# Kernel optimization log

Hardware: AMD Instinct MI355X
Metric: run time of the kernel (lower is better)

## Reference

```python
import jax, jax.numpy as jnp
import numpy as np

D_DEC, D_ENC, H, D_MLP = 1024, 768, 16, 4096
HD = D_DEC // H


def _layernorm(x, w, b, eps=1e-5):
    m = x.mean(-1, keepdims=True)
    v = ((x - m) ** 2).mean(-1, keepdims=True)
    return (x - m) / jnp.sqrt(v + eps) * w + b


def setup_inputs() -> dict:
    key = jax.random.key(0)
    ks = jax.random.split(key, 16)
    B, T, S = 4, 1024, 576

    def lin(k, din, dout):
        kw, kb = jax.random.split(k)
        bound = 1.0 / np.sqrt(din)
        W = jax.random.uniform(kw, (din, dout), jnp.float32, -bound, bound)
        b = jax.random.uniform(kb, (dout,), jnp.float32, -bound, bound)
        return W, b

    qkv_w, qkv_b = lin(ks[0], D_DEC, 3 * D_DEC)
    proj_w, proj_b = lin(ks[1], D_DEC, D_DEC)
    q_w, q_b = lin(ks[2], D_DEC, D_DEC)
    k_w, k_b = lin(ks[3], D_ENC, D_DEC)
    v_w, v_b = lin(ks[4], D_ENC, D_DEC)
    out_w, out_b = lin(ks[5], D_DEC, D_DEC)
    mlp1_w, mlp1_b = lin(ks[6], D_DEC, D_MLP)
    mlp2_w, mlp2_b = lin(ks[7], D_MLP, D_DEC)

    return {
        "x": jax.random.normal(ks[8], (B, T, D_DEC), jnp.float32),
        "enc": jax.random.normal(ks[9], (B, S, D_ENC), jnp.float32),
        "tgt_key_padding_mask": jnp.zeros((B, T), bool),
        "enc_padding_mask": jnp.zeros((B, S), bool),
        "ln1_w": jnp.ones((D_DEC,)), "ln1_b": jnp.zeros((D_DEC,)),
        "qkv_w": qkv_w, "qkv_b": qkv_b, "proj_w": proj_w, "proj_b": proj_b,
        "ln2_w": jnp.ones((D_DEC,)), "ln2_b": jnp.zeros((D_DEC,)),
        "q_w": q_w, "q_b": q_b, "k_w": k_w, "k_b": k_b,
        "v_w": v_w, "v_b": v_b, "out_w": out_w, "out_b": out_b,
        "ln3_w": jnp.ones((D_DEC,)), "ln3_b": jnp.zeros((D_DEC,)),
        "mlp1_w": mlp1_w, "mlp1_b": mlp1_b, "mlp2_w": mlp2_w, "mlp2_b": mlp2_b,
    }


def _decoder_block(x, enc, tgt_mask, enc_mask,
                   ln1_w, ln1_b, qkv_w, qkv_b, proj_w, proj_b,
                   ln2_w, ln2_b, q_w, q_b, k_w, k_b, v_w, v_b, out_w, out_b,
                   ln3_w, ln3_b, mlp1_w, mlp1_b, mlp2_w, mlp2_b):
    B, T, C = x.shape
    S = enc.shape[1]
    scale = HD ** -0.5
    neg = jnp.asarray(-jnp.inf, x.dtype)

    # ---- causal self-attention ----
    h = _layernorm(x, ln1_w, ln1_b)
    qkv = (h @ qkv_w + qkv_b).reshape(B, T, 3, H, HD)
    q, k, v = [qkv[:, :, i].transpose(0, 2, 1, 3) for i in range(3)]  # [B,H,T,HD]
    attn = jnp.einsum("bhtd,bhsd->bhts", q, k) * scale
    causal = jnp.triu(jnp.ones((T, T), bool), 1)
    attn = jnp.where(causal[None, None], neg, attn)
    attn = jnp.where(tgt_mask[:, None, None, :], neg, attn)
    attn = jax.nn.softmax(attn, axis=-1)
    sa = jnp.einsum("bhts,bhsd->bhtd", attn, v).transpose(0, 2, 1, 3).reshape(B, T, C)
    x = x + sa @ proj_w + proj_b

    # ---- cross-attention ----
    h = _layernorm(x, ln2_w, ln2_b)
    q = (h @ q_w + q_b).reshape(B, T, H, HD).transpose(0, 2, 1, 3)
    k = (enc @ k_w + k_b).reshape(B, S, H, HD).transpose(0, 2, 1, 3)
    v = (enc @ v_w + v_b).reshape(B, S, H, HD).transpose(0, 2, 1, 3)
    attn = jnp.einsum("bhtd,bhsd->bhts", q, k) * scale
    attn = jnp.where(enc_mask[:, None, None, :], neg, attn)
    attn = jax.nn.softmax(attn, axis=-1)
    ca = jnp.einsum("bhts,bhsd->bhtd", attn, v).transpose(0, 2, 1, 3).reshape(B, T, C)
    x = x + ca @ out_w + out_b

    # ---- MLP (exact GELU, matching torch nn.GELU default) ----
    h = _layernorm(x, ln3_w, ln3_b)
    h = jax.nn.gelu(h @ mlp1_w + mlp1_b, approximate=False)
    x = x + h @ mlp2_w + mlp2_b
    return x


def reference(x, enc, tgt_key_padding_mask, enc_padding_mask,
              ln1_w, ln1_b, qkv_w, qkv_b, proj_w, proj_b,
              ln2_w, ln2_b, q_w, q_b, k_w, k_b, v_w, v_b, out_w, out_b,
              ln3_w, ln3_b, mlp1_w, mlp1_b, mlp2_w, mlp2_b):
    return _decoder_block(x, enc, tgt_key_padding_mask, enc_padding_mask,
                          ln1_w, ln1_b, qkv_w, qkv_b, proj_w, proj_b,
                          ln2_w, ln2_b, q_w, q_b, k_w, k_b, v_w, v_b, out_w, out_b,
                          ln3_w, ln3_b, mlp1_w, mlp1_b, mlp2_w, mlp2_b)
```

## Files before the change

kernel.cpp:

```cpp
#include <hip/hip_runtime.h>
#include <hip/hip_bf16.h>

typedef unsigned short u16;
typedef __bf16 bf16x8 __attribute__((ext_vector_type(8)));
typedef float f32x4 __attribute__((ext_vector_type(4)));

__device__ __forceinline__ float bf2f(u16 v) { return __uint_as_float(((unsigned)v) << 16); }
__device__ __forceinline__ u16 f2bf(float f) {
  unsigned u = __float_as_uint(f);
  u += 0x7FFFu + ((u >> 16) & 1u);
  return (u16)(u >> 16);
}
__device__ __forceinline__ float gelu_exact(float x) {
  return 0.5f * x * (1.0f + erff(x * 0.70710678118654752f));
}

__device__ __forceinline__ void async_load16(const u16* g, u16* l) {
  __builtin_amdgcn_global_load_lds((const __attribute__((address_space(1))) void*)g,
                                   (__attribute__((address_space(3))) void*)l, 16, 0, 0);
}

__global__ void sniff_kernel(const u16* __restrict__ x, int* __restrict__ flag) {
  int tid = threadIdx.x;
  int hits = 0;
  #pragma unroll
  for (int s = 0; s < 2; ++s) {
    float f = fabsf(bf2f(x[2 * (tid + 64 * s)]));
    hits += (f >= 0.00390625f && f <= 16.0f) ? 1 : 0;
  }
  #pragma unroll
  for (int off = 32; off; off >>= 1) hits += __shfl_xor(hits, off);
  if (tid == 0) flag[0] = (hits >= 64) ? 1 : 0;
}

__global__ __launch_bounds__(256) void in2bf_kernel(const void* __restrict__ src, u16* __restrict__ dst,
                                                    int n4, const int* __restrict__ flagp) {
  int i = blockIdx.x * 256 + threadIdx.x;
  if (i >= n4) return;
  if (*flagp) {
    ((ushort4*)dst)[i] = ((const ushort4*)src)[i];
  } else {
    float4 v = ((const float4*)src)[i];
    ushort4 o; o.x = f2bf(v.x); o.y = f2bf(v.y); o.z = f2bf(v.z); o.w = f2bf(v.w);
    ((ushort4*)dst)[i] = o;
  }
}

__global__ __launch_bounds__(256) void small2bf_kernel(
    const void* s0, const void* s1, const void* s2, const void* s3,
    const void* s4, const void* s5, const void* s6, const void* s7,
    const void* s8, const void* s9, const void* s10, const void* s11,
    const void* s12, const void* s13,
    u16* __restrict__ dst, const int* __restrict__ flagp) {
  const void* srcs[14] = {s0, s1, s2, s3, s4, s5, s6, s7, s8, s9, s10, s11, s12, s13};
  int blk = blockIdx.x;
  int seg, u;
  if (blk < 6)       { seg = blk;            u = 0; }
  else if (blk < 9)  { seg = 6;              u = blk - 6; }
  else if (blk < 14) { seg = 7 + (blk - 9);  u = 0; }
  else if (blk < 18) { seg = 12;             u = blk - 14; }
  else               { seg = 13;             u = 0; }
  const void* src = srcs[seg];
  int i = threadIdx.x + u * 256;
  u16* d = dst + (size_t)blk * 1024;
  if (*flagp) {
    ((ushort4*)d)[threadIdx.x] = ((const ushort4*)src)[i];
  } else {
    float4 v = ((const float4*)src)[i];
    ushort4 o; o.x = f2bf(v.x); o.y = f2bf(v.y); o.z = f2bf(v.z); o.w = f2bf(v.w);
    ((ushort4*)d)[threadIdx.x] = o;
  }
}

__global__ __launch_bounds__(256) void in2f32_kernel(const void* __restrict__ src, float* __restrict__ dst,
                                                     int n4, const int* __restrict__ flagp) {
  int i = blockIdx.x * 256 + threadIdx.x;
  if (i >= n4) return;
  if (*flagp) {
    ushort4 v = ((const ushort4*)src)[i];
    float4 o; o.x = bf2f(v.x); o.y = bf2f(v.y); o.z = bf2f(v.z); o.w = bf2f(v.w);
    ((float4*)dst)[i] = o;
  } else {
    ((float4*)dst)[i] = ((const float4*)src)[i];
  }
}

__global__ __launch_bounds__(256) void transpose_k(const void* __restrict__ in_, u16* __restrict__ out,
                                                   int R, int C, const int* __restrict__ flagp) {
  int flag = *flagp;
  __shared__ u16 tile[32][33];
  int c0 = blockIdx.x * 32, r0 = blockIdx.y * 32;
  int tx = threadIdx.x & 31, ty = threadIdx.x >> 5;
  #pragma unroll
  for (int j = 0; j < 32; j += 8) {
    size_t idx = (size_t)(r0 + ty + j) * C + c0 + tx;
    tile[ty + j][tx] = flag ? ((const u16*)in_)[idx] : f2bf(((const float*)in_)[idx]);
  }
  __syncthreads();
  #pragma unroll
  for (int j = 0; j < 32; j += 8)
    out[(size_t)(c0 + ty + j) * R + r0 + tx] = tile[tx][ty + j];
}

__global__ __launch_bounds__(256) void ln_kernel(const float* __restrict__ x,
                                                 const u16* __restrict__ w, const u16* __restrict__ b,
                                                 u16* __restrict__ out) {
  int row = blockIdx.x, tid = threadIdx.x;
  float4 v = ((const float4*)(x + (size_t)row * 1024))[tid];
  float s = v.x + v.y + v.z + v.w;
  #pragma unroll
  for (int off = 32; off; off >>= 1) s += __shfl_xor(s, off);
  __shared__ float red1[4], red2[4];
  if ((tid & 63) == 0) red1[tid >> 6] = s;
  __syncthreads();
  float mean = (red1[0] + red1[1] + red1[2] + red1[3]) * (1.0f / 1024.0f);
  float d0 = v.x - mean, d1 = v.y - mean, d2 = v.z - mean, d3 = v.w - mean;
  float vs = d0 * d0 + d1 * d1 + d2 * d2 + d3 * d3;
  #pragma unroll
  for (int off = 32; off; off >>= 1) vs += __shfl_xor(vs, off);
  if ((tid & 63) == 0) red2[tid >> 6] = vs;
  __syncthreads();
  float var = (red2[0] + red2[1] + red2[2] + red2[3]) * (1.0f / 1024.0f);
  float rs = rsqrtf(var + 1e-5f);
  int c = tid * 4;
  ushort4 o;
  o.x = f2bf(d0 * rs * bf2f(w[c + 0]) + bf2f(b[c + 0]));
  o.y = f2bf(d1 * rs * bf2f(w[c + 1]) + bf2f(b[c + 1]));
  o.z = f2bf(d2 * rs * bf2f(w[c + 2]) + bf2f(b[c + 2]));
  o.w = f2bf(d3 * rs * bf2f(w[c + 3]) + bf2f(b[c + 3]));
  ((ushort4*)(out + (size_t)row * 1024))[tid] = o;
}

template <int MODE, int TN>
__global__ __launch_bounds__(256) void gemm_tn(const u16* __restrict__ A, const u16* __restrict__ Bt,
                                               const u16* __restrict__ bias,
                                               const float* __restrict__ resid_in, float* __restrict__ resid_out,
                                               void* __restrict__ outp, int M, int N, int K,
                                               const int* __restrict__ flagp) {
  constexpr int NI = TN / 32;
  __shared__ __align__(16) u16 As[128 * 64];
  __shared__ __align__(16) u16 Bs[TN * 64];

  int nwg = gridDim.x * gridDim.y;
  int bid = blockIdx.y * gridDim.x + blockIdx.x;
  int chunk = nwg >> 3;
  int s = (bid & 7) * chunk + (bid >> 3);
  int bx = s % gridDim.x, by = s / gridDim.x;

  int n0 = bx * TN, m0 = by * 128;
  int tid = threadIdx.x;
  int lane = tid & 63, w = tid >> 6;
  int wm = w & 1, wn = w >> 1;
  int quad = lane >> 4, l15 = lane & 15;
  int sw = l15 & 7;
  int flag = (MODE == 3) ? *flagp : 0;
  f32x4 acc[4][NI];
  #pragma unroll
  for (int i = 0; i < 4; i++)
    #pragma unroll
    for (int j = 0; j < NI; j++) acc[i][j] = (f32x4){0.f, 0.f, 0.f, 0.f};

  int srow8 = lane >> 3;
  int scol = ((lane & 7) ^ srow8) * 8;
  const u16* Abase = A + (size_t)(m0 + srow8) * K + scol;
  const u16* Bbase = Bt + (size_t)(n0 + srow8) * K + scol;

  for (int k0 = 0; k0 < K; k0 += 64) {
    #pragma unroll
    for (int j = 0; j < 4; ++j) {
      int r0 = (w * 4 + j) * 8;
      async_load16(Abase + (size_t)r0 * K + k0, &As[r0 * 64]);
    }
    #pragma unroll
    for (int j = 0; j < TN / 32; ++j) {
      int r0 = (w * (TN / 32) + j) * 8;
      async_load16(Bbase + (size_t)r0 * K + k0, &Bs[r0 * 64]);
    }
    __syncthreads();
    #pragma unroll
    for (int kk = 0; kk < 64; kk += 32) {
      int cbase = (kk >> 3) + quad;
      int slot = (cbase ^ sw) << 3;
      bf16x8 af[4], bfr[NI];
      #pragma unroll
      for (int i = 0; i < 4; i++)
        af[i] = *(const bf16x8*)&As[(wm * 64 + i * 16 + l15) * 64 + slot];
      #pragma unroll
      for (int j = 0; j < NI; j++)
        bfr[j] = *(const bf16x8*)&Bs[(wn * (TN / 2) + j * 16 + l15) * 64 + slot];
      #pragma unroll
      for (int mi = 0; mi < 4; mi++)
        #pragma unroll
        for (int ni = 0; ni < NI; ni++)
          acc[mi][ni] = __builtin_amdgcn_mfma_f32_16x16x32_bf16(af[mi], bfr[ni], acc[mi][ni], 0, 0, 0);
    }
    __syncthreads();
  }

  int col_base = n0 + wn * (TN / 2), row_base = m0 + wm * 64;
  #pragma unroll
  for (int mi = 0; mi < 4; mi++) {
    #pragma unroll
    for (int ni = 0; ni < NI; ni++) {
      int col = col_base + ni * 16 + l15;
      float bv = bf2f(bias[col]);
      #pragma unroll
      for (int r = 0; r < 4; r++) {
        int row = row_base + mi * 16 + quad * 4 + r;
        float vv = acc[mi][ni][r] + bv;
        size_t idx = (size_t)row * N + col;
        if (MODE == 0) ((u16*)outp)[idx] = f2bf(vv);
        else if (MODE == 1) resid_out[idx] = resid_in[idx] + vv;
        else if (MODE == 2) ((u16*)outp)[idx] = f2bf(gelu_exact(vv));
        else {
          float ov = resid_in[idx] + vv;
          if (flag) ((u16*)outp)[idx] = f2bf(ov);
          else ((float*)outp)[idx] = ov;
        }
      }
    }
  }
}

__global__ __launch_bounds__(256) void attn_mfma(const u16* __restrict__ Q, const u16* __restrict__ K,
                                                 const u16* __restrict__ V, u16* __restrict__ O,
                                                 int T, int S, int qstride, int kstride, int causal) {
  int bh = blockIdx.y, b = bh >> 4, h = bh & 15;
  int gx = gridDim.x, xi = blockIdx.x;
  int qi = (xi & 1) ? (gx - 1 - (xi >> 1)) : (xi >> 1);
  int qt = qi * 64;

  const u16* Qb = Q + (size_t)b * T * qstride + h * 64;
  const u16* Kb = K + (size_t)b * S * kstride + h * 64;
  const u16* Vb = V + (size_t)b * S * kstride + h * 64;
  u16* Ob = O + (size_t)b * T * 1024 + h * 64;

  int tid = threadIdx.x, lane = tid & 63, w = tid >> 6;
  int quad = lane >> 4, l15 = lane & 15;

  __shared__ __align__(16) u16 Ks[64 * 64];
  __shared__ __align__(16) u16 Vt[64 * 64];
  __shared__ __align__(16) u16 Ps[4][16 * 64];

  int srow8 = lane >> 3;
  int scol = ((lane & 7) ^ srow8) * 8;

  #pragma unroll
  for (int j = 0; j < 2; ++j) {
    int r0 = (w * 2 + j) * 8;
    async_load16(Qb + (size_t)(qt + r0 + srow8) * qstride + scol, &Ks[r0 * 64]);
  }
  asm volatile("" ::: "memory");
  uint4 v0 = *(const uint4*)&Vb[(size_t)lane * kstride + w * 16];
  uint4 v1 = *(const uint4*)&Vb[(size_t)lane * kstride + w * 16 + 8];
  asm volatile("s_waitcnt vmcnt(2)" ::: "memory");
  __builtin_amdgcn_s_barrier();

  int qrow = w * 16 + l15;
  bf16x8 qfrag[2];
  #pragma unroll
  for (int c = 0; c < 2; ++c)
    qfrag[c] = *(const bf16x8*)&Ks[qrow * 64 + (((c * 4 + quad) ^ (l15 & 7)) << 3)];
  asm volatile("s_waitcnt lgkmcnt(0)" ::: "memory");

  float m_i[4], l_i[4];
  f32x4 oacc[4];
  #pragma unroll
  for (int r = 0; r < 4; ++r) { m_i[r] = -1e30f; l_i[r] = 0.f; }
  #pragma unroll
  for (int ni = 0; ni < 4; ++ni) oacc[ni] = (f32x4){0.f, 0.f, 0.f, 0.f};

  int nk = causal ? (qi + 1) * 64 : S;
  int tg0 = qt + w * 16 + quad * 4;

  for (int s0 = 0; s0 < nk; s0 += 64) {
    __builtin_amdgcn_s_barrier();
    #pragma unroll
    for (int j = 0; j < 2; ++j) {
      int r0 = (w * 2 + j) * 8;
      async_load16(Kb + (size_t)(s0 + r0 + srow8) * kstride + scol, &Ks[r0 * 64]);
    }
    asm volatile("" ::: "memory");
    union { uint4 u[2]; u16 e[16]; } vv; vv.u[0] = v0; vv.u[1] = v1;
    #pragma unroll
    for (int j = 0; j < 16; ++j) {
      int d = w * 16 + j;
      Vt[d * 64 + ((((lane >> 3) ^ (j & 7)) << 3) | (lane & 7))] = vv.e[j];
    }
    if (s0 + 64 < nk) {
      v0 = *(const uint4*)&Vb[(size_t)(s0 + 64 + lane) * kstride + w * 16];
      v1 = *(const uint4*)&Vb[(size_t)(s0 + 64 + lane) * kstride + w * 16 + 8];
      asm volatile("s_waitcnt vmcnt(2)" ::: "memory");
    } else {
      asm volatile("s_waitcnt vmcnt(0)" ::: "memory");
    }
    asm volatile("s_waitcnt lgkmcnt(0)" ::: "memory");
    __builtin_amdgcn_s_barrier();

    f32x4 sacc[4];
    #pragma unroll
    for (int ni = 0; ni < 4; ++ni) sacc[ni] = (f32x4){0.f, 0.f, 0.f, 0.f};
    __builtin_amdgcn_s_setprio(1);
    #pragma unroll
    for (int c = 0; c < 2; ++c) {
      #pragma unroll
      for (int ni = 0; ni < 4; ++ni) {
        bf16x8 kf = *(const bf16x8*)&Ks[(ni * 16 + l15) * 64 + (((c * 4 + quad) ^ (l15 & 7)) << 3)];
        sacc[ni] = __builtin_amdgcn_mfma_f32_16x16x32_bf16(qfrag[c], kf, sacc[ni], 0, 0, 0);
      }
    }
    __builtin_amdgcn_s_setprio(0);

    #pragma unroll
    for (int ni = 0; ni < 4; ++ni)
      #pragma unroll
      for (int r = 0; r < 4; ++r) sacc[ni][r] *= 0.125f;
    if (causal && s0 + 63 > qt + w * 16) {
      #pragma unroll
      for (int ni = 0; ni < 4; ++ni) {
        int key = s0 + ni * 16 + l15;
        #pragma unroll
        for (int r = 0; r < 4; ++r)
          if (key > tg0 + r) sacc[ni][r] = -1e30f;
      }
    }

    float mnew[4], alpha[4], psum[4];
    #pragma unroll
    for (int r = 0; r < 4; ++r) {
      float mx = fmaxf(fmaxf(sacc[0][r], sacc[1][r]), fmaxf(sacc[2][r], sacc[3][r]));
      #pragma unroll
      for (int off = 1; off < 16; off <<= 1) mx = fmaxf(mx, __shfl_xor(mx, off));
      mnew[r] = fmaxf(m_i[r], mx);
      alpha[r] = __expf(m_i[r] - mnew[r]);
      m_i[r] = mnew[r];
      psum[r] = 0.f;
    }
    #pragma unroll
    for (int ni = 0; ni < 4; ++ni) {
      #pragma unroll
      for (int r = 0; r < 4; ++r) {
        float p = __expf(sacc[ni][r] - mnew[r]);
        psum[r] += p;
        int row = quad * 4 + r;
        int blk = (ni * 2 + (l15 >> 3)) ^ (row & 7);
        Ps[w][row * 64 + (blk << 3) + (l15 & 7)] = f2bf(p);
      }
    }
    #pragma unroll
    for (int r = 0; r < 4; ++r) {
      float ps = psum[r];
      #pragma unroll
      for (int off = 1; off < 16; off <<= 1) ps += __shfl_xor(ps, off);
      l_i[r] = l_i[r] * alpha[r] + ps;
    }

    bf16x8 pfrag[2];
    #pragma unroll
    for (int c = 0; c < 2; ++c)
      pfrag[c] = *(const bf16x8*)&Ps[w][l15 * 64 + (((c * 4 + quad) ^ (l15 & 7)) << 3)];
    #pragma unroll
    for (int ni = 0; ni < 4; ++ni)
      #pragma unroll
      for (int r = 0; r < 4; ++r) oacc[ni][r] *= alpha[r];
    __builtin_amdgcn_s_setprio(1);
    #pragma unroll
    for (int c = 0; c < 2; ++c) {
      #pragma unroll
      for (int ni = 0; ni < 4; ++ni) {
        bf16x8 vf = *(const bf16x8*)&Vt[(ni * 16 + l15) * 64 + (((c * 4 + quad) ^ (l15 & 7)) << 3)];
        oacc[ni] = __builtin_amdgcn_mfma_f32_16x16x32_bf16(pfrag[c], vf, oacc[ni], 0, 0, 0);
      }
    }
    __builtin_amdgcn_s_setprio(0);
  }

  #pragma unroll
  for (int ni = 0; ni < 4; ++ni) {
    #pragma unroll
    for (int r = 0; r < 4; ++r) {
      int t = tg0 + r;
      int d = ni * 16 + l15;
      Ob[(size_t)t * 1024 + d] = f2bf(oacc[ni][r] / l_i[r]);
    }
  }
}

extern "C" void kernel_launch(void* const* d_in, const int* in_sizes, int n_in,
                              void* d_out, int out_size, void* d_ws, size_t ws_size,
                              hipStream_t stream) {
  const void* x_in   = d_in[0];
  const void* enc_in = d_in[1];
  const void* ln1_w = d_in[4];  const void* ln1_b = d_in[5];
  const void* qkv_w = d_in[6];  const void* qkv_b = d_in[7];
  const void* proj_w = d_in[8]; const void* proj_b = d_in[9];
  const void* ln2_w = d_in[10]; const void* ln2_b = d_in[11];
  const void* q_w = d_in[12];   const void* q_b = d_in[13];
  const void* k_w = d_in[14];   const void* k_b = d_in[15];
  const void* v_w = d_in[16];   const void* v_b = d_in[17];
  const void* out_w = d_in[18]; const void* out_b = d_in[19];
  const void* ln3_w = d_in[20]; const void* ln3_b = d_in[21];
  const void* mlp1_w = d_in[22]; const void* mlp1_b = d_in[23];
  const void* mlp2_w = d_in[24]; const void* mlp2_b = d_in[25];

  char* ws = (char*)d_ws;
  size_t off = 0;
  auto alloc = [&](size_t bytes) { char* p = ws + off; off += (bytes + 255) & ~(size_t)255; return p; };
  float* xf   = (float*)alloc(4096ull * 1024 * 4);
  u16* hb     = (u16*)alloc(4096ull * 1024 * 2);
  u16* big    = (u16*)alloc(4096ull * 4096 * 2);
  u16* wT     = (u16*)alloc(3072ull * 1024 * 2);
  u16* encb   = (u16*)alloc(2304ull * 768 * 2);
  u16* pool   = (u16*)alloc(20480ull * 2);
  int* flag   = (int*)alloc(256);
  (void)ws_size;

  u16* q_bf = big;
  u16* k_bf = big + 4096ull * 1024;
  u16* v_bf = big + (4096ull + 2304) * 1024;

  u16 *p_ln1w = pool, *p_ln1b = pool + 1024, *p_ln2w = pool + 2048, *p_ln2b = pool + 3072;
  u16 *p_ln3w = pool + 4096, *p_ln3b = pool + 5120;
  u16 *p_qkvb = pool + 6144, *p_projb = pool + 9216, *p_qb = pool + 10240, *p_kb = pool + 11264;
  u16 *p_vb = pool + 12288, *p_outb = pool + 13312, *p_m1b = pool + 14336, *p_m2b = pool + 18432;

  sniff_kernel<<<1, 64, 0, stream>>>((const u16*)x_in, flag);
  in2f32_kernel<<<4096, 256, 0, stream>>>(x_in, xf, 1048576, flag);
  in2bf_kernel<<<1728, 256, 0, stream>>>(enc_in, encb, 442368, flag);
  small2bf_kernel<<<19, 256, 0, stream>>>(ln1_w, ln1_b, ln2_w, ln2_b, ln3_w, ln3_b,
                                          qkv_b, proj_b, q_b, k_b, v_b, out_b,
                                          mlp1_b, mlp2_b, pool, flag);

  ln_kernel<<<4096, 256, 0, stream>>>(xf, p_ln1w, p_ln1b, hb);
  transpose_k<<<dim3(96, 32), 256, 0, stream>>>(qkv_w, wT, 1024, 3072, flag);
  gemm_tn<0, 128><<<dim3(24, 32), 256, 0, stream>>>(hb, wT, p_qkvb, nullptr, nullptr, big, 4096, 3072, 1024, flag);
  attn_mfma<<<dim3(16, 64), 256, 0, stream>>>(big, big + 1024, big + 2048, hb, 1024, 1024, 3072, 3072, 1);
  transpose_k<<<dim3(32, 32), 256, 0, stream>>>(proj_w, wT, 1024, 1024, flag);
  gemm_tn<1, 64><<<dim3(16, 32), 256, 0, stream>>>(hb, wT, p_projb, xf, xf, nullptr, 4096, 1024, 1024, flag);

  ln_kernel<<<4096, 256, 0, stream>>>(xf, p_ln2w, p_ln2b, hb);
  transpose_k<<<dim3(32, 32), 256, 0, stream>>>(q_w, wT, 1024, 1024, flag);
  gemm_tn<0, 64><<<dim3(16, 32), 256, 0, stream>>>(hb, wT, p_qb, nullptr, nullptr, q_bf, 4096, 1024, 1024, flag);
  transpose_k<<<dim3(32, 24), 256, 0, stream>>>(k_w, wT, 768, 1024, flag);
  gemm_tn<0, 64><<<dim3(16, 18), 256, 0, stream>>>(encb, wT, p_kb, nullptr, nullptr, k_bf, 2304, 1024, 768, flag);
  transpose_k<<<dim3(32, 24), 256, 0, stream>>>(v_w, wT, 768, 1024, flag);
  gemm_tn<0, 64><<<dim3(16, 18), 256, 0, stream>>>(encb, wT, p_vb, nullptr, nullptr, v_bf, 2304, 1024, 768, flag);
  attn_mfma<<<dim3(16, 64), 256, 0, stream>>>(q_bf, k_bf, v_bf, hb, 1024, 576, 1024, 1024, 0);
  transpose_k<<<dim3(32, 32), 256, 0, stream>>>(out_w, wT, 1024, 1024, flag);
  gemm_tn<1, 64><<<dim3(16, 32), 256, 0, stream>>>(hb, wT, p_outb, xf, xf, nullptr, 4096, 1024, 1024, flag);

  ln_kernel<<<4096, 256, 0, stream>>>(xf, p_ln3w, p_ln3b, hb);
  transpose_k<<<dim3(128, 32), 256, 0, stream>>>(mlp1_w, wT, 1024, 4096, flag);
  gemm_tn<2, 128><<<dim3(32, 32), 256, 0, stream>>>(hb, wT, p_m1b, nullptr, nullptr, big, 4096, 4096, 1024, flag);
  transpose_k<<<dim3(32, 128), 256, 0, stream>>>(mlp2_w, wT, 4096, 1024, flag);
  gemm_tn<3, 64><<<dim3(16, 32), 256, 0, stream>>>(big, wT, p_m2b, xf, nullptr, d_out, 4096, 1024, 4096, flag);
}
```

Before: 589.0 us.

## Process 128 query rows per attention block to reuse K/V tiles

Each attention workgroup now handles two 64-row query blocks (128 rows), so every K and V tile loaded into shared memory serves twice as many queries, halving K/V load and transpose traffic. The grid drops to 8 blocks along x, causal scheduling switches to a diagonal rotation of query tiles, and the first row block is skipped once it is fully masked. This costs more registers (launch bounds set to 2 blocks per SM), a larger P buffer in LDS, and fewer blocks in flight.

```diff
diff --git a/kernel.cpp b/kernel.cpp
--- a/kernel.cpp
+++ b/kernel.cpp
@@ -222,13 +222,13 @@
   }
 }
 
-__global__ __launch_bounds__(256) void attn_mfma(const u16* __restrict__ Q, const u16* __restrict__ K,
-                                                 const u16* __restrict__ V, u16* __restrict__ O,
-                                                 int T, int S, int qstride, int kstride, int causal) {
+__global__ __launch_bounds__(256, 2) void attn_mfma(const u16* __restrict__ Q, const u16* __restrict__ K,
+                                                    const u16* __restrict__ V, u16* __restrict__ O,
+                                                    int T, int S, int qstride, int kstride, int causal) {
   int bh = blockIdx.y, b = bh >> 4, h = bh & 15;
-  int gx = gridDim.x, xi = blockIdx.x;
-  int qi = (xi & 1) ? (gx - 1 - (xi >> 1)) : (xi >> 1);
-  int qt = qi * 64;
+  int x = blockIdx.x, y = blockIdx.y;
+  int qi = causal ? ((x + y) & 7) : x;
+  int qt = qi * 128;
 
   const u16* Qb = Q + (size_t)b * T * qstride + h * 64;
   const u16* Kb = K + (size_t)b * S * kstride + h * 64;
@@ -240,15 +240,15 @@
 
   __shared__ __align__(16) u16 Ks[64 * 64];
   __shared__ __align__(16) u16 Vt[64 * 64];
-  __shared__ __align__(16) u16 Ps[4][16 * 64];
+  __shared__ __align__(16) u16 Ps[128 * 64];
 
   int srow8 = lane >> 3;
   int scol = ((lane & 7) ^ srow8) * 8;
 
   #pragma unroll
-  for (int j = 0; j < 2; ++j) {
-    int r0 = (w * 2 + j) * 8;
-    async_load16(Qb + (size_t)(qt + r0 + srow8) * qstride + scol, &Ks[r0 * 64]);
+  for (int j = 0; j < 4; ++j) {
+    int r0 = (w * 4 + j) * 8;
+    async_load16(Qb + (size_t)(qt + r0 + srow8) * qstride + scol, &Ps[r0 * 64]);
   }
   asm volatile("" ::: "memory");
   uint4 v0 = *(const uint4*)&Vb[(size_t)lane * kstride + w * 16];
@@ -256,22 +256,25 @@
   asm volatile("s_waitcnt vmcnt(2)" ::: "memory");
   __builtin_amdgcn_s_barrier();
 
-  int qrow = w * 16 + l15;
-  bf16x8 qfrag[2];
-  #pragma unroll
-  for (int c = 0; c < 2; ++c)
-    qfrag[c] = *(const bf16x8*)&Ks[qrow * 64 + (((c * 4 + quad) ^ (l15 & 7)) << 3)];
+  bf16x8 qfrag[2][2];
+  #pragma unroll
+  for (int rb = 0; rb < 2; ++rb)
+    #pragma unroll
+    for (int c = 0; c < 2; ++c)
+      qfrag[rb][c] = *(const bf16x8*)&Ps[(rb * 64 + w * 16 + l15) * 64 + (((c * 4 + quad) ^ (l15 & 7)) << 3)];
   asm volatile("s_waitcnt lgkmcnt(0)" ::: "memory");
 
-  float m_i[4], l_i[4];
-  f32x4 oacc[4];
-  #pragma unroll
-  for (int r = 0; r < 4; ++r) { m_i[r] = -1e30f; l_i[r] = 0.f; }
-  #pragma unroll
-  for (int ni = 0; ni < 4; ++ni) oacc[ni] = (f32x4){0.f, 0.f, 0.f, 0.f};
-
-  int nk = causal ? (qi + 1) * 64 : S;
-  int tg0 = qt + w * 16 + quad * 4;
+  float m_i[2][4], l_i[2][4];
+  f32x4 oacc[2][4];
+  #pragma unroll
+  for (int rb = 0; rb < 2; ++rb) {
+    #pragma unroll
+    for (int r = 0; r < 4; ++r) { m_i[rb][r] = -1e30f; l_i[rb][r] = 0.f; }
+    #pragma unroll
+    for (int ni = 0; ni < 4; ++ni) oacc[rb][ni] = (f32x4){0.f, 0.f, 0.f, 0.f};
+  }
+
+  int nk = causal ? (qt + 128) : S;
 
   for (int s0 = 0; s0 < nk; s0 += 64) {
     __builtin_amdgcn_s_barrier();
@@ -297,91 +300,101 @@
     asm volatile("s_waitcnt lgkmcnt(0)" ::: "memory");
     __builtin_amdgcn_s_barrier();
 
-    f32x4 sacc[4];
-    #pragma unroll
-    for (int ni = 0; ni < 4; ++ni) sacc[ni] = (f32x4){0.f, 0.f, 0.f, 0.f};
-    __builtin_amdgcn_s_setprio(1);
-    #pragma unroll
-    for (int c = 0; c < 2; ++c) {
+    #pragma unroll
+    for (int rb = 0; rb < 2; ++rb) {
+      if (rb == 0 && causal && s0 >= qt + 64) continue;
+      int tg0 = qt + rb * 64 + w * 16 + quad * 4;
+
+      f32x4 sacc[4];
+      #pragma unroll
+      for (int ni = 0; ni < 4; ++ni) sacc[ni] = (f32x4){0.f, 0.f, 0.f, 0.f};
+      __builtin_amdgcn_s_setprio(1);
+      #pragma unroll
+      for (int c = 0; c < 2; ++c) {
+        #pragma unroll
+        for (int ni = 0; ni < 4; ++ni) {
+          bf16x8 kf = *(const bf16x8*)&Ks[(ni * 16 + l15) * 64 + (((c * 4 + quad) ^ (l15 & 7)) << 3)];
+          sacc[ni] = __builtin_amdgcn_mfma_f32_16x16x32_bf16(qfrag[rb][c], kf, sacc[ni], 0, 0, 0);
+        }
+      }
+      __builtin_amdgcn_s_setprio(0);
+
+      #pragma unroll
+      for (int ni = 0; ni < 4; ++ni)
+        #pragma unroll
+        for (int r = 0; r < 4; ++r) sacc[ni][r] *= 0.125f;
+      if (causal && s0 + 63 > qt + rb * 64 + w * 16) {
+        #pragma unroll
+        for (int ni = 0; ni < 4; ++ni) {
+          int key = s0 + ni * 16 + l15;
+          #pragma unroll
+          for (int r = 0; r < 4; ++r)
+            if (key > tg0 + r) sacc[ni][r] = -1e30f;
+        }
+      }
+
+      float mnew[4], alpha[4], psum[4];
+      #pragma unroll
+      for (int r = 0; r < 4; ++r) {
+        float mx = fmaxf(fmaxf(sacc[0][r], sacc[1][r]), fmaxf(sacc[2][r], sacc[3][r]));
+        #pragma unroll
+        for (int off = 1; off < 16; off <<= 1) mx = fmaxf(mx, __shfl_xor(mx, off));
+        mnew[r] = fmaxf(m_i[rb][r], mx);
+        alpha[r] = __expf(m_i[rb][r] - mnew[r]);
+        m_i[rb][r] = mnew[r];
+        psum[r] = 0.f;
+      }
       #pragma unroll
       for (int ni = 0; ni < 4; ++ni) {
-        bf16x8 kf = *(const bf16x8*)&Ks[(ni * 16 + l15) * 64 + (((c * 4 + quad) ^ (l15 & 7)) << 3)];
-        sacc[ni] = __builtin_amdgcn_mfma_f32_16x16x32_bf16(qfrag[c], kf, sacc[ni], 0, 0, 0);
-      }
-    }
-    __builtin_amdgcn_s_setprio(0);
-
-    #pragma unroll
-    for (int ni = 0; ni < 4; ++ni)
-      #pragma unroll
-      for (int r = 0; r < 4; ++r) sacc[ni][r] *= 0.125f;
-    if (causal && s0 + 63 > qt + w * 16) {
-      #pragma unroll
-      for (int ni = 0; ni < 4; ++ni) {
-        int key = s0 + ni * 16 + l15;
-        #pragma unroll
-        for (int r = 0; r < 4; ++r)
-          if (key > tg0 + r) sacc[ni][r] = -1e30f;
-      }
-    }
-
-    float mnew[4], alpha[4], psum[4];
-    #pragma unroll
-    for (int r = 0; r < 4; ++r) {
-      float mx = fmaxf(fmaxf(sacc[0][r], sacc[1][r]), fmaxf(sacc[2][r], sacc[3][r]));
-      #pragma unroll
-      for (int off = 1; off < 16; off <<= 1) mx = fmaxf(mx, __shfl_xor(mx, off));
-      mnew[r] = fmaxf(m_i[r], mx);
-      alpha[r] = __expf(m_i[r] - mnew[r]);
-      m_i[r] = mnew[r];
-      psum[r] = 0.f;
-    }
+        #pragma unroll
+        for (int r = 0; r < 4; ++r) {
+          float p = __expf(sacc[ni][r] - mnew[r]);
+          psum[r] += p;
+          int row = quad * 4 + r;
+          int blk = (ni * 2 + (l15 >> 3)) ^ (row & 7);
+          Ps[(w * 32 + rb * 16 + row) * 64 + (blk << 3) + (l15 & 7)] = f2bf(p);
+        }
+      }
+      #pragma unroll
+      for (int r = 0; r < 4; ++r) {
+        float ps = psum[r];
+        #pragma unroll
+        for (int off = 1; off < 16; off <<= 1) ps += __shfl_xor(ps, off);
+        l_i[rb][r] = l_i[rb][r] * alpha[r] + ps;
+      }
+
+      bf16x8 pfrag[2];
+      #pragma unroll
+      for (int c = 0; c < 2; ++c)
+        pfrag[c] = *(const bf16x8*)&Ps[(w * 32 + rb * 16 + l15) * 64 + (((c * 4 + quad) ^ (l15 & 7)) << 3)];
+      #pragma unroll
+      for (int ni = 0; ni < 4; ++ni)
+        #pragma unroll
+        for (int r = 0; r < 4; ++r) oacc[rb][ni][r] *= alpha[r];
+      __builtin_amdgcn_s_setprio(1);
+      #pragma unroll
+      for (int c = 0; c < 2; ++c) {
+        #pragma unroll
+        for (int ni = 0; ni < 4; ++ni) {
+          bf16x8 vf = *(const bf16x8*)&Vt[(ni * 16 + l15) * 64 + (((c * 4 + quad) ^ (l15 & 7)) << 3)];
+          oacc[rb][ni] = __builtin_amdgcn_mfma_f32_16x16x32_bf16(pfrag[c], vf, oacc[rb][ni], 0, 0, 0);
+        }
+      }
+      __builtin_amdgcn_s_setprio(0);
+    }
+  }
+
+  #pragma unroll
+  for (int rb = 0; rb < 2; ++rb) {
+    int tg0 = qt + rb * 64 + w * 16 + quad * 4;
     #pragma unroll
     for (int ni = 0; ni < 4; ++ni) {
       #pragma unroll
       for (int r = 0; r < 4; ++r) {
-        float p = __expf(sacc[ni][r] - mnew[r]);
-        psum[r] += p;
-        int row = quad * 4 + r;
-        int blk = (ni * 2 + (l15 >> 3)) ^ (row & 7);
-        Ps[w][row * 64 + (blk << 3) + (l15 & 7)] = f2bf(p);
-      }
-    }
-    #pragma unroll
-    for (int r = 0; r < 4; ++r) {
-      float ps = psum[r];
-      #pragma unroll
-      for (int off = 1; off < 16; off <<= 1) ps += __shfl_xor(ps, off);
-      l_i[r] = l_i[r] * alpha[r] + ps;
-    }
-
-    bf16x8 pfrag[2];
-    #pragma unroll
-    for (int c = 0; c < 2; ++c)
-      pfrag[c] = *(const bf16x8*)&Ps[w][l15 * 64 + (((c * 4 + quad) ^ (l15 & 7)) << 3)];
-    #pragma unroll
-    for (int ni = 0; ni < 4; ++ni)
-      #pragma unroll
-      for (int r = 0; r < 4; ++r) oacc[ni][r] *= alpha[r];
-    __builtin_amdgcn_s_setprio(1);
-    #pragma unroll
-    for (int c = 0; c < 2; ++c) {
-      #pragma unroll
-      for (int ni = 0; ni < 4; ++ni) {
-        bf16x8 vf = *(const bf16x8*)&Vt[(ni * 16 + l15) * 64 + (((c * 4 + quad) ^ (l15 & 7)) << 3)];
-        oacc[ni] = __builtin_amdgcn_mfma_f32_16x16x32_bf16(pfrag[c], vf, oacc[ni], 0, 0, 0);
-      }
-    }
-    __builtin_amdgcn_s_setprio(0);
-  }
-
-  #pragma unroll
-  for (int ni = 0; ni < 4; ++ni) {
-    #pragma unroll
-    for (int r = 0; r < 4; ++r) {
-      int t = tg0 + r;
-      int d = ni * 16 + l15;
-      Ob[(size_t)t * 1024 + d] = f2bf(oacc[ni][r] / l_i[r]);
+        int t = tg0 + r;
+        int d = ni * 16 + l15;
+        Ob[(size_t)t * 1024 + d] = f2bf(oacc[rb][ni][r] / l_i[rb][r]);
+      }
     }
   }
 }
@@ -434,7 +447,7 @@
   ln_kernel<<<4096, 256, 0, stream>>>(xf, p_ln1w, p_ln1b, hb);
   transpose_k<<<dim3(96, 32), 256, 0, stream>>>(qkv_w, wT, 1024, 3072, flag);
   gemm_tn<0, 128><<<dim3(24, 32), 256, 0, stream>>>(hb, wT, p_qkvb, nullptr, nullptr, big, 4096, 3072, 1024, flag);
-  attn_mfma<<<dim3(16, 64), 256, 0, stream>>>(big, big + 1024, big + 2048, hb, 1024, 1024, 3072, 3072, 1);
+  attn_mfma<<<dim3(8, 64), 256, 0, stream>>>(big, big + 1024, big + 2048, hb, 1024, 1024, 3072, 3072, 1);
   transpose_k<<<dim3(32, 32), 256, 0, stream>>>(proj_w, wT, 1024, 1024, flag);
   gemm_tn<1, 64><<<dim3(16, 32), 256, 0, stream>>>(hb, wT, p_projb, xf, xf, nullptr, 4096, 1024, 1024, flag);
 
@@ -445,7 +458,7 @@
   gemm_tn<0, 64><<<dim3(16, 18), 256, 0, stream>>>(encb, wT, p_kb, nullptr, nullptr, k_bf, 2304, 1024, 768, flag);
   transpose_k<<<dim3(32, 24), 256, 0, stream>>>(v_w, wT, 768, 1024, flag);
   gemm_tn<0, 64><<<dim3(16, 18), 256, 0, stream>>>(encb, wT, p_vb, nullptr, nullptr, v_bf, 2304, 1024, 768, flag);
-  attn_mfma<<<dim3(16, 64), 256, 0, stream>>>(q_bf, k_bf, v_bf, hb, 1024, 576, 1024, 1024, 0);
+  attn_mfma<<<dim3(8, 64), 256, 0, stream>>>(q_bf, k_bf, v_bf, hb, 1024, 576, 1024, 1024, 0);
   transpose_k<<<dim3(32, 32), 256, 0, stream>>>(out_w, wT, 1024, 1024, flag);
   gemm_tn<1, 64><<<dim3(16, 32), 256, 0, stream>>>(hb, wT, p_outb, xf, xf, nullptr, 4096, 1024, 1024, flag);
 
```

Result: no change. 577.5 us (-2.0%).

## Add 256x128 eight-wave GEMM with XCD-aware block remap; remap attention grid

Applied to the files above, without the earlier changes.

Adds a gemm_wide kernel with 512 threads and a 256x128 output tile, which doubles A-tile reuse. Block IDs are remapped so consecutive chunks stay on the same XCD for better L2 locality. It replaces the QKV and MLP1 GEMMs. The attention kernel also gets an XCD-aware mapping that groups heads per chunk, in place of the old alternating causal load-balancing order. The new GEMM has no double buffering and uses a full sync per K step, so latency hiding may suffer, and the attention change may unbalance the causal work.

```diff
diff --git a/kernel.cpp b/kernel.cpp
--- a/kernel.cpp
+++ b/kernel.cpp
@@ -222,12 +222,95 @@
   }
 }
 
+template <int MODE>
+__global__ __launch_bounds__(512) void gemm_wide(const u16* __restrict__ A, const u16* __restrict__ Bt,
+                                                 const u16* __restrict__ bias,
+                                                 void* __restrict__ outp, int M, int N, int K) {
+  __shared__ __align__(16) u16 As[256 * 64];
+  __shared__ __align__(16) u16 Bs[128 * 64];
+
+  int nwg = gridDim.x * gridDim.y;
+  int bid = blockIdx.y * gridDim.x + blockIdx.x;
+  int chunk = nwg >> 3;
+  int s = (bid & 7) * chunk + (bid >> 3);
+  int bx = s % gridDim.x, by = s / gridDim.x;
+
+  int n0 = bx * 128, m0 = by * 256;
+  int tid = threadIdx.x;
+  int lane = tid & 63, w = tid >> 6;
+  int wm = w & 3, wn = w >> 2;
+  int quad = lane >> 4, l15 = lane & 15;
+  int sw = l15 & 7;
+  f32x4 acc[4][4];
+  #pragma unroll
+  for (int i = 0; i < 4; i++)
+    #pragma unroll
+    for (int j = 0; j < 4; j++) acc[i][j] = (f32x4){0.f, 0.f, 0.f, 0.f};
+
+  int srow8 = lane >> 3;
+  int scol = ((lane & 7) ^ srow8) * 8;
+  const u16* Abase = A + (size_t)(m0 + srow8) * K + scol;
+  const u16* Bbase = Bt + (size_t)(n0 + srow8) * K + scol;
+
+  for (int k0 = 0; k0 < K; k0 += 64) {
+    #pragma unroll
+    for (int j = 0; j < 4; ++j) {
+      int r0 = (w * 4 + j) * 8;
+      async_load16(Abase + (size_t)r0 * K + k0, &As[r0 * 64]);
+    }
+    #pragma unroll
+    for (int j = 0; j < 2; ++j) {
+      int r0 = (w * 2 + j) * 8;
+      async_load16(Bbase + (size_t)r0 * K + k0, &Bs[r0 * 64]);
+    }
+    __syncthreads();
+    #pragma unroll
+    for (int kk = 0; kk < 64; kk += 32) {
+      int cbase = (kk >> 3) + quad;
+      int slot = (cbase ^ sw) << 3;
+      bf16x8 af[4], bfr[4];
+      #pragma unroll
+      for (int i = 0; i < 4; i++)
+        af[i] = *(const bf16x8*)&As[(wm * 64 + i * 16 + l15) * 64 + slot];
+      #pragma unroll
+      for (int j = 0; j < 4; j++)
+        bfr[j] = *(const bf16x8*)&Bs[(wn * 64 + j * 16 + l15) * 64 + slot];
+      #pragma unroll
+      for (int mi = 0; mi < 4; mi++)
+        #pragma unroll
+        for (int ni = 0; ni < 4; ni++)
+          acc[mi][ni] = __builtin_amdgcn_mfma_f32_16x16x32_bf16(af[mi], bfr[ni], acc[mi][ni], 0, 0, 0);
+    }
+    __syncthreads();
+  }
+
+  int col_base = n0 + wn * 64, row_base = m0 + wm * 64;
+  #pragma unroll
+  for (int mi = 0; mi < 4; mi++) {
+    #pragma unroll
+    for (int ni = 0; ni < 4; ni++) {
+      int col = col_base + ni * 16 + l15;
+      float bv = bf2f(bias[col]);
+      #pragma unroll
+      for (int r = 0; r < 4; r++) {
+        int row = row_base + mi * 16 + quad * 4 + r;
+        float vv = acc[mi][ni][r] + bv;
+        size_t idx = (size_t)row * N + col;
+        if (MODE == 0) ((u16*)outp)[idx] = f2bf(vv);
+        else ((u16*)outp)[idx] = f2bf(gelu_exact(vv));
+      }
+    }
+  }
+}
+
 __global__ __launch_bounds__(256) void attn_mfma(const u16* __restrict__ Q, const u16* __restrict__ K,
                                                  const u16* __restrict__ V, u16* __restrict__ O,
                                                  int T, int S, int qstride, int kstride, int causal) {
-  int bh = blockIdx.y, b = bh >> 4, h = bh & 15;
-  int gx = gridDim.x, xi = blockIdx.x;
-  int qi = (xi & 1) ? (gx - 1 - (xi >> 1)) : (xi >> 1);
+  int slot = blockIdx.y * gridDim.x + blockIdx.x;
+  int c = slot & 7, u = slot >> 3;
+  int bh = c * 8 + (u >> 4);
+  int qi = u & 15;
+  int b = bh >> 4, h = bh & 15;
   int qt = qi * 64;
 
   const u16* Qb = Q + (size_t)b * T * qstride + h * 64;
@@ -259,8 +342,8 @@
   int qrow = w * 16 + l15;
   bf16x8 qfrag[2];
   #pragma unroll
-  for (int c = 0; c < 2; ++c)
-    qfrag[c] = *(const bf16x8*)&Ks[qrow * 64 + (((c * 4 + quad) ^ (l15 & 7)) << 3)];
+  for (int cc = 0; cc < 2; ++cc)
+    qfrag[cc] = *(const bf16x8*)&Ks[qrow * 64 + (((cc * 4 + quad) ^ (l15 & 7)) << 3)];
   asm volatile("s_waitcnt lgkmcnt(0)" ::: "memory");
 
   float m_i[4], l_i[4];
@@ -281,7 +364,7 @@
       async_load16(Kb + (size_t)(s0 + r0 + srow8) * kstride + scol, &Ks[r0 * 64]);
     }
     asm volatile("" ::: "memory");
-    union { uint4 u[2]; u16 e[16]; } vv; vv.u[0] = v0; vv.u[1] = v1;
+    union { uint4 u4[2]; u16 e[16]; } vv; vv.u4[0] = v0; vv.u4[1] = v1;
     #pragma unroll
     for (int j = 0; j < 16; ++j) {
       int d = w * 16 + j;
@@ -302,11 +385,11 @@
     for (int ni = 0; ni < 4; ++ni) sacc[ni] = (f32x4){0.f, 0.f, 0.f, 0.f};
     __builtin_amdgcn_s_setprio(1);
     #pragma unroll
-    for (int c = 0; c < 2; ++c) {
+    for (int cc = 0; cc < 2; ++cc) {
       #pragma unroll
       for (int ni = 0; ni < 4; ++ni) {
-        bf16x8 kf = *(const bf16x8*)&Ks[(ni * 16 + l15) * 64 + (((c * 4 + quad) ^ (l15 & 7)) << 3)];
-        sacc[ni] = __builtin_amdgcn_mfma_f32_16x16x32_bf16(qfrag[c], kf, sacc[ni], 0, 0, 0);
+        bf16x8 kf = *(const bf16x8*)&Ks[(ni * 16 + l15) * 64 + (((cc * 4 + quad) ^ (l15 & 7)) << 3)];
+        sacc[ni] = __builtin_amdgcn_mfma_f32_16x16x32_bf16(qfrag[cc], kf, sacc[ni], 0, 0, 0);
       }
     }
     __builtin_amdgcn_s_setprio(0);
@@ -357,19 +440,19 @@
 
     bf16x8 pfrag[2];
     #pragma unroll
-    for (int c = 0; c < 2; ++c)
-      pfrag[c] = *(const bf16x8*)&Ps[w][l15 * 64 + (((c * 4 + quad) ^ (l15 & 7)) << 3)];
+    for (int cc = 0; cc < 2; ++cc)
+      pfrag[cc] = *(const bf16x8*)&Ps[w][l15 * 64 + (((cc * 4 + quad) ^ (l15 & 7)) << 3)];
     #pragma unroll
     for (int ni = 0; ni < 4; ++ni)
       #pragma unroll
       for (int r = 0; r < 4; ++r) oacc[ni][r] *= alpha[r];
     __builtin_amdgcn_s_setprio(1);
     #pragma unroll
-    for (int c = 0; c < 2; ++c) {
+    for (int cc = 0; cc < 2; ++cc) {
       #pragma unroll
       for (int ni = 0; ni < 4; ++ni) {
-        bf16x8 vf = *(const bf16x8*)&Vt[(ni * 16 + l15) * 64 + (((c * 4 + quad) ^ (l15 & 7)) << 3)];
-        oacc[ni] = __builtin_amdgcn_mfma_f32_16x16x32_bf16(pfrag[c], vf, oacc[ni], 0, 0, 0);
+        bf16x8 vf = *(const bf16x8*)&Vt[(ni * 16 + l15) * 64 + (((cc * 4 + quad) ^ (l15 & 7)) << 3)];
+        oacc[ni] = __builtin_amdgcn_mfma_f32_16x16x32_bf16(pfrag[cc], vf, oacc[ni], 0, 0, 0);
       }
     }
     __builtin_amdgcn_s_setprio(0);
@@ -433,7 +516,7 @@
 
   ln_kernel<<<4096, 256, 0, stream>>>(xf, p_ln1w, p_ln1b, hb);
   transpose_k<<<dim3(96, 32), 256, 0, stream>>>(qkv_w, wT, 1024, 3072, flag);
-  gemm_tn<0, 128><<<dim3(24, 32), 256, 0, stream>>>(hb, wT, p_qkvb, nullptr, nullptr, big, 4096, 3072, 1024, flag);
+  gemm_wide<0><<<dim3(24, 16), 512, 0, stream>>>(hb, wT, p_qkvb, big, 4096, 3072, 1024);
   attn_mfma<<<dim3(16, 64), 256, 0, stream>>>(big, big + 1024, big + 2048, hb, 1024, 1024, 3072, 3072, 1);
   transpose_k<<<dim3(32, 32), 256, 0, stream>>>(proj_w, wT, 1024, 1024, flag);
   gemm_tn<1, 64><<<dim3(16, 32), 256, 0, stream>>>(hb, wT, p_projb, xf, xf, nullptr, 4096, 1024, 1024, flag);
@@ -451,7 +534,7 @@
 
   ln_kernel<<<4096, 256, 0, stream>>>(xf, p_ln3w, p_ln3b, hb);
   transpose_k<<<dim3(128, 32), 256, 0, stream>>>(mlp1_w, wT, 1024, 4096, flag);
-  gemm_tn<2, 128><<<dim3(32, 32), 256, 0, stream>>>(hb, wT, p_m1b, nullptr, nullptr, big, 4096, 4096, 1024, flag);
+  gemm_wide<2><<<dim3(32, 16), 512, 0, stream>>>(hb, wT, p_m1b, big, 4096, 4096, 1024);
   transpose_k<<<dim3(32, 128), 256, 0, stream>>>(mlp2_w, wT, 4096, 1024, flag);
   gemm_tn<3, 64><<<dim3(16, 32), 256, 0, stream>>>(big, wT, p_m2b, xf, nullptr, d_out, 4096, 1024, 4096, flag);
 }
```

New measurement: 533.6 us. -9.4%, faster.
